# Kernel tuning notes

Measured on AMD Instinct MI355X. Metric: run time of the kernel, lower is better.

## Reference

```python
import jax, jax.numpy as jnp
import numpy as np

N_NODES = 20000
N_EDGES = 120000
N_GRAPHS = 512
F_IN = 300
NHID = 256
NHID_FF = 256
NOUT = 768
SLOPE = 0.2
EPS = 1e-16


def _p(key, shape, scale=0.05):
    return jax.random.normal(key, shape, dtype=jnp.float32) * scale


def setup_inputs() -> dict:
    key = jax.random.key(0)
    ks = jax.random.split(key, 24)
    inp = {
        "x": jax.random.normal(ks[0], (N_NODES, F_IN), dtype=jnp.float32),
        "edge_index": jax.random.randint(ks[1], (2, N_EDGES), 0, N_NODES, dtype=jnp.int64) if False else jax.random.randint(ks[1], (2, N_EDGES), 0, N_NODES).astype(jnp.int32),
        "batch": jnp.sort(jax.random.randint(ks[2], (N_NODES,), 0, N_GRAPHS)).astype(jnp.int32),
        # conv1: in=300 -> heads=4, C=256, concat
        "c1_wl": _p(ks[3], (4 * NHID, F_IN)),
        "c1_wr": _p(ks[4], (4 * NHID, F_IN)),
        "c1_att": _p(ks[5], (4, NHID)),
        "c1_b": jnp.zeros((4 * NHID,), jnp.float32),
        # conv2: in=1024 -> heads=4, C=256, concat
        "c2_wl": _p(ks[6], (4 * NHID, 4 * NHID)),
        "c2_wr": _p(ks[7], (4 * NHID, 4 * NHID)),
        "c2_att": _p(ks[8], (4, NHID)),
        "c2_b": jnp.zeros((4 * NHID,), jnp.float32),
        # conv3: in=1024 -> heads=6, C=256, mean (concat=False)
        "c3_wl": _p(ks[9], (6 * NHID_FF, 4 * NHID)),
        "c3_wr": _p(ks[10], (6 * NHID_FF, 4 * NHID)),
        "c3_att": _p(ks[11], (6, NHID_FF)),
        "c3_b": jnp.zeros((NHID_FF,), jnp.float32),
        # post-process MLP
        "fp1_w": _p(ks[12], (NHID_FF, NHID_FF)),
        "fp1_b": jnp.zeros((NHID_FF,), jnp.float32),
        "fp2_w": _p(ks[13], (NOUT, NHID_FF)),
        "fp2_b": jnp.zeros((NOUT,), jnp.float32),
    }
    return inp


def gatv2(x, src, dst, wl, wr, att, b, concat):
    """GATv2Conv (PyG semantics, eval mode): lin_l on source, lin_r on target,
    score = att . leaky_relu(xl_j + xr_i), segment softmax over dst, aggregate xl_j."""
    n = x.shape[0]
    H, C = att.shape
    xl = (x @ wl.T).reshape(n, H, C)
    xr = (x @ wr.T).reshape(n, H, C)
    s = xl[src] + xr[dst]                                   # [E,H,C] gather
    s = jnp.where(s > 0, s, SLOPE * s)                      # leaky_relu
    scores = jnp.einsum("ehc,hc->eh", s, att)               # [E,H]
    mx = jax.ops.segment_max(scores, dst, num_segments=n)   # [N,H]
    ex = jnp.exp(scores - mx[dst])
    denom = jax.ops.segment_sum(ex, dst, num_segments=n)
    alpha = ex / (denom[dst] + EPS)                         # [E,H]
    out = jax.ops.segment_sum(alpha[:, :, None] * xl[src], dst, num_segments=n)  # [N,H,C]
    out = out.reshape(n, H * C) if concat else out.mean(axis=1)
    return out + b


def reference(x, edge_index, batch, c1_wl, c1_wr, c1_att, c1_b,
              c2_wl, c2_wr, c2_att, c2_b, c3_wl, c3_wr, c3_att, c3_b,
              fp1_w, fp1_b, fp2_w, fp2_b):
    n = x.shape[0]
    # PyG GATv2Conv defaults add_self_loops=True
    loops = jnp.arange(n, dtype=edge_index.dtype)
    src = jnp.concatenate([edge_index[0], loops])
    dst = jnp.concatenate([edge_index[1], loops])

    h = jax.nn.elu(gatv2(x, src, dst, c1_wl, c1_wr, c1_att, c1_b, concat=True))
    h = jax.nn.elu(gatv2(h, src, dst, c2_wl, c2_wr, c2_att, c2_b, concat=True))
    h = gatv2(h, src, dst, c3_wl, c3_wr, c3_att, c3_b, concat=False)

    # F.normalize(p=2, dim=-1), torch eps=1e-12
    norm = jnp.linalg.norm(h, axis=-1, keepdims=True)
    h = h / jnp.maximum(norm, 1e-12)

    # global_mean_pool over `batch`
    sums = jax.ops.segment_sum(h, batch, num_segments=N_GRAPHS)
    cnts = jax.ops.segment_sum(jnp.ones((n,), h.dtype), batch, num_segments=N_GRAPHS)
    pooled = sums / jnp.maximum(cnts, 1.0)[:, None]

    h = jax.nn.relu(pooled @ fp1_w.T + fp1_b)
    return h @ fp2_w.T + fp2_b
```

## Files before the change

kernel.cpp:

```cpp
#include <hip/hip_runtime.h>

typedef _Float16 h16;
typedef _Float16 h16x2 __attribute__((ext_vector_type(2)));
typedef _Float16 h16x4 __attribute__((ext_vector_type(4)));
typedef _Float16 h16x8 __attribute__((ext_vector_type(8)));
typedef float f32x4 __attribute__((ext_vector_type(4)));

static constexpr int NN   = 20000;
static constexpr int NPAD = 20224;
static constexpr int NE0  = 120000;
static constexpr int NE   = 140000;
static constexpr int NG   = 512;
static constexpr int FIN  = 300;
static constexpr int K1P  = 384;
static constexpr int CD   = 256;
static constexpr float SLOPE = 0.2f;

#define GLDS16(gsrc, ldst)                                                              \
  __builtin_amdgcn_global_load_lds(                                                    \
      (const __attribute__((address_space(1))) unsigned int*)(gsrc),                    \
      (__attribute__((address_space(3))) unsigned int*)(ldst), 16, 0, 0)

__global__ __launch_bounds__(256) void fill_x_kernel(const float* __restrict__ x, h16* __restrict__ a1) {
  int r = blockIdx.x;
  for (int c = threadIdx.x; c < K1P; c += 256) {
    float v = (r < NN && c < FIN) ? x[(size_t)r * FIN + c] : 0.f;
    a1[(size_t)r * K1P + c] = (h16)v;
  }
}

__global__ __launch_bounds__(256) void conv_w2_kernel(const float* __restrict__ wl, const float* __restrict__ wr,
                                                      h16* __restrict__ o, int rows, int cols, int colsp) {
  int r = blockIdx.x;
  const float* s = (r < rows) ? (wl + (size_t)r * cols) : (wr + (size_t)(r - rows) * cols);
  for (int c = threadIdx.x; c < colsp; c += 256) {
    float v = (c < cols) ? s[c] : 0.f;
    o[(size_t)r * colsp + c] = (h16)v;
  }
}

__global__ __launch_bounds__(256) void attcvt_kernel(const float* __restrict__ a, h16* __restrict__ o, int n) {
  int i = blockIdx.x * 256 + threadIdx.x;
  if (i < n) o[i] = (h16)a[i];
}

__global__ __launch_bounds__(256) void build_edges_kernel(const int* __restrict__ ei,
                                                          int* __restrict__ src, int* __restrict__ dst) {
  int e = blockIdx.x * 256 + threadIdx.x;
  if (e >= NE) return;
  if (e < NE0) { src[e] = ei[e]; dst[e] = ei[NE0 + e]; }
  else         { src[e] = e - NE0; dst[e] = e - NE0; }
}

__global__ __launch_bounds__(256) void deg_kernel(const int* __restrict__ dst, int* __restrict__ deg) {
  int e = blockIdx.x * 256 + threadIdx.x;
  if (e < NE) atomicAdd(&deg[dst[e]], 1);
}

__global__ __launch_bounds__(1024) void scan_kernel(const int* __restrict__ deg, int* __restrict__ rowptr) {
  __shared__ int b0[1024], b1[1024];
  __shared__ int carry;
  int t = threadIdx.x;
  if (t == 0) carry = 0;
  __syncthreads();
  for (int base = 0; base < NN; base += 1024) {
    int x = (base + t < NN) ? deg[base + t] : 0;
    b0[t] = x;
    __syncthreads();
    int* cur = b0; int* nxt = b1;
    for (int off = 1; off < 1024; off <<= 1) {
      int v = cur[t];
      if (t >= off) v += cur[t - off];
      nxt[t] = v;
      __syncthreads();
      int* tmp = cur; cur = nxt; nxt = tmp;
    }
    if (base + t < NN) rowptr[base + t] = carry + cur[t] - x;
    __syncthreads();
    if (t == 0) carry += cur[1023];
    __syncthreads();
  }
  if (t == 0) rowptr[NN] = carry;
}

__global__ __launch_bounds__(256) void scatter_kernel(const int* __restrict__ src, const int* __restrict__ dst,
                                                      const int* __restrict__ rowptr, int* __restrict__ cursor,
                                                      int* __restrict__ esrc) {
  int e = blockIdx.x * 256 + threadIdx.x;
  if (e >= NE) return;
  int d = dst[e];
  int pos = rowptr[d] + atomicAdd(&cursor[d], 1);
  esrc[pos] = src[e];
}

__global__ __launch_bounds__(512, 2) void gemm256_kernel(const h16* __restrict__ A, const h16* __restrict__ B,
                                                         h16* __restrict__ Co, int K, int Nw, int ntN) {
  __shared__ __align__(16) h16 lds[4 * 16384];
  int nwg = gridDim.x;
  int q = nwg >> 3, r = nwg & 7;
  int xc = blockIdx.x & 7, idx = blockIdx.x >> 3;
  int logical = (xc < r ? xc * (q + 1) : r * (q + 1) + (xc - r) * q) + idx;
  int tm = (logical / ntN) * 256, tn = (logical % ntN) * 256;

  int tid = threadIdx.x;
  int wv = tid >> 6, lane = tid & 63;
  int wm = (wv >> 2) * 128, wn = (wv & 3) * 64;
  int lrow = lane & 15, kq = lane >> 4, lr7 = lrow & 7;

  int rowoff = tid >> 3;
  int ug = ((tid & 7) ^ (rowoff & 7)) * 8;
  int ldsoff = (tid >> 6) * 512;

  const int NT = K >> 6;

  auto STAGE = [&](int buf, int kt) {
#pragma unroll
    for (int j = 0; j < 4; ++j) {
      GLDS16(A + (size_t)(tm + j * 64 + rowoff) * K + kt * 64 + ug,
             &lds[(buf * 2 + 0) * 16384 + j * 4096 + ldsoff]);
      GLDS16(B + (size_t)(tn + j * 64 + rowoff) * K + kt * 64 + ug,
             &lds[(buf * 2 + 1) * 16384 + j * 4096 + ldsoff]);
    }
  };

  STAGE(0, 0);
  STAGE(1, 1);

  f32x4 acc[8][4] = {};
  for (int t = 0; t < NT; ++t) {
    int b = t & 1;
    if (t + 1 < NT) { asm volatile("s_waitcnt vmcnt(8)" ::: "memory"); }
    else            { asm volatile("s_waitcnt vmcnt(0)" ::: "memory"); }
    __builtin_amdgcn_s_barrier();

    const h16* As_ = &lds[(b * 2 + 0) * 16384];
    const h16* Bs_ = &lds[(b * 2 + 1) * 16384];
    h16x8 af[8], bf[4];
#pragma unroll
    for (int i = 0; i < 8; ++i) af[i] = *(const h16x8*)&As_[(wm + i * 16 + lrow) * 64 + ((kq ^ lr7) * 8)];
#pragma unroll
    for (int j = 0; j < 4; ++j) bf[j] = *(const h16x8*)&Bs_[(wn + j * 16 + lrow) * 64 + ((kq ^ lr7) * 8)];
#pragma unroll
    for (int i = 0; i < 8; ++i)
#pragma unroll
      for (int j = 0; j < 4; ++j)
        acc[i][j] = __builtin_amdgcn_mfma_f32_16x16x32_f16(af[i], bf[j], acc[i][j], 0, 0, 0);
#pragma unroll
    for (int i = 0; i < 8; ++i) af[i] = *(const h16x8*)&As_[(wm + i * 16 + lrow) * 64 + (((4 + kq) ^ lr7) * 8)];
#pragma unroll
    for (int j = 0; j < 4; ++j) bf[j] = *(const h16x8*)&Bs_[(wn + j * 16 + lrow) * 64 + (((4 + kq) ^ lr7) * 8)];
    asm volatile("s_waitcnt lgkmcnt(0)" ::: "memory");
    __builtin_amdgcn_sched_barrier(0);
    __builtin_amdgcn_s_barrier();
    if (t + 2 < NT) STAGE(b, t + 2);
    __builtin_amdgcn_s_setprio(1);
#pragma unroll
    for (int i = 0; i < 8; ++i)
#pragma unroll
      for (int j = 0; j < 4; ++j)
        acc[i][j] = __builtin_amdgcn_mfma_f32_16x16x32_f16(af[i], bf[j], acc[i][j], 0, 0, 0);
    __builtin_amdgcn_s_setprio(0);
  }

  int cr = kq * 4, cc = lrow;
#pragma unroll
  for (int i = 0; i < 8; ++i)
#pragma unroll
    for (int j = 0; j < 4; ++j) {
      size_t base = (size_t)(tm + wm + i * 16 + cr) * Nw + (tn + wn + j * 16 + cc);
#pragma unroll
      for (int qq = 0; qq < 4; qq++) Co[base + (size_t)qq * Nw] = (h16)acc[i][j][qq];
    }
}

template <int H, int MODE>
__global__ __launch_bounds__(64 * H) void sagg_kernel(
    const h16* __restrict__ X, const int* __restrict__ rowptr, const int* __restrict__ esrc,
    const h16* __restrict__ attH, const float* __restrict__ bias,
    h16* __restrict__ outA, const int* __restrict__ batch,
    float* __restrict__ pooled, int* __restrict__ cnt) {
  constexpr int NS = H / 2;
  constexpr int HC = H * CD;
  constexpr unsigned ROWB = (unsigned)(4 * HC);
  int tid = threadIdx.x;
  int w = tid >> 6, lane = tid & 63;
  int k = w / NS, s = w - k * NS;
  int n = blockIdx.x * 2 + k;
  unsigned sby = (unsigned)s * 1024u + (unsigned)lane * 16u;
  const char* Xb = (const char*)X;
  unsigned nrow = (unsigned)n * ROWB;

  h16x8 xr8 = *(const h16x8*)(Xb + nrow + (unsigned)(2 * HC) + sby);
  h16x8 aw8 = *(const h16x8*)((const char*)attH + sby);
  int beg = rowptr[n], end = rowptr[n + 1];

  float m = -1e30f, den = 0.f;
  float acc[8] = {0.f, 0.f, 0.f, 0.f, 0.f, 0.f, 0.f, 0.f};

  for (int i = beg; i < end; i += 8) {
    int cn = end - i; if (cn > 8) cn = 8;
    unsigned offs[8];
#pragma unroll
    for (int kk = 0; kk < 8; ++kk) {
      int idx = i + kk; if (idx > end - 1) idx = end - 1;
      offs[kk] = (unsigned)esrc[idx] * ROWB + sby;
    }
    h16x8 xv[8];
#pragma unroll
    for (int kk = 0; kk < 8; ++kk) xv[kk] = *(const h16x8*)(Xb + offs[kk]);
    float ps[8];
#pragma unroll
    for (int kk = 0; kk < 8; ++kk) {
      h16x8 v = xv[kk] + xr8;
      h16x8 u = v * (h16)SLOPE;
      v = __builtin_elementwise_max(v, u);
      float p = 0.f;
      p = __builtin_amdgcn_fdot2(__builtin_shufflevector(v, v, 0, 1),
                                 __builtin_shufflevector(aw8, aw8, 0, 1), p, false);
      p = __builtin_amdgcn_fdot2(__builtin_shufflevector(v, v, 2, 3),
                                 __builtin_shufflevector(aw8, aw8, 2, 3), p, false);
      p = __builtin_amdgcn_fdot2(__builtin_shufflevector(v, v, 4, 5),
                                 __builtin_shufflevector(aw8, aw8, 4, 5), p, false);
      p = __builtin_amdgcn_fdot2(__builtin_shufflevector(v, v, 6, 7),
                                 __builtin_shufflevector(aw8, aw8, 6, 7), p, false);
      p += __shfl_xor(p, 1);  p += __shfl_xor(p, 2);  p += __shfl_xor(p, 4);
      p += __shfl_xor(p, 8);  p += __shfl_xor(p, 16);
      ps[kk] = p;
    }
    float pm = ps[0];
#pragma unroll
    for (int kk = 1; kk < 8; ++kk) pm = fmaxf(pm, ps[kk]);
    float nm = fmaxf(m, pm);
    float f = __expf(m - nm);
    den *= f;
#pragma unroll
    for (int j = 0; j < 8; ++j) acc[j] *= f;
#pragma unroll
    for (int kk = 0; kk < 8; ++kk) {
      float we = (kk < cn) ? __expf(ps[kk] - nm) : 0.f;
      den += we;
#pragma unroll
      for (int j = 0; j < 8; ++j) acc[j] += we * (float)xv[kk][j];
    }
    m = nm;
  }
  float inv = 1.f / (den + 1e-16f);

  if (MODE == 0) {
    const float* bp = bias + s * 512 + lane * 8;
    float4 b0 = *(const float4*)bp;
    float4 b1 = *(const float4*)(bp + 4);
    const float* bb = (const float*)&b0;
    const float* bb2 = (const float*)&b1;
    h16x8 ov;
#pragma unroll
    for (int j = 0; j < 8; ++j) {
      float o = acc[j] * inv + (j < 4 ? bb[j] : bb2[j - 4]);
      o = o > 0.f ? o : expm1f(o);
      ov[j] = (h16)o;
    }
    *(h16x8*)(outA + (unsigned)n * HC + s * 512 + lane * 8) = ov;
  } else {
    __shared__ float sacc[2][NS][32][8];
    __shared__ float spart[2][2 * NS];
    float t8[8];
#pragma unroll
    for (int j = 0; j < 8; ++j) {
      t8[j] = acc[j] * inv;
      t8[j] += __shfl_xor(t8[j], 32);
    }
    if (lane < 32) {
#pragma unroll
      for (int j = 0; j < 8; ++j) sacc[k][s][lane][j] = t8[j];
    }
    __syncthreads();
#pragma unroll
    for (int kk = 0; kk < 2; ++kk) {
      float mv = 0.f;
      if (tid < CD) {
#pragma unroll
        for (int s2 = 0; s2 < NS; ++s2) mv += sacc[kk][s2][tid >> 3][tid & 7];
        mv = mv * (1.f / H) + bias[tid];
      }
      float ss = (tid < CD) ? mv * mv : 0.f;
      ss += __shfl_xor(ss, 1);  ss += __shfl_xor(ss, 2);  ss += __shfl_xor(ss, 4);
      ss += __shfl_xor(ss, 8);  ss += __shfl_xor(ss, 16); ss += __shfl_xor(ss, 32);
      if (lane == 0) spart[kk][w] = ss;
      __syncthreads();
      float tot = 0.f;
#pragma unroll
      for (int ww = 0; ww < 2 * NS; ++ww) tot += spart[kk][ww];
      float scale = 1.f / fmaxf(sqrtf(tot), 1e-12f);
      int g = batch[blockIdx.x * 2 + kk];
      if (tid < CD) atomicAdd(&pooled[(unsigned)g * CD + tid], mv * scale);
      if (tid == 0) atomicAdd(&cnt[g], 1);
    }
  }
}

__global__ __launch_bounds__(256) void pool_div_kernel(float* __restrict__ pooled, const int* __restrict__ cnt) {
  int g = blockIdx.x, t = threadIdx.x;
  pooled[(size_t)g * CD + t] /= fmaxf((float)cnt[g], 1.f);
}

__global__ __launch_bounds__(256) void mlp1_kernel(const float* __restrict__ pooled, const float* __restrict__ w,
                                                   const float* __restrict__ b, float* __restrict__ hid) {
  __shared__ float xs[CD];
  int g = blockIdx.x, t = threadIdx.x;
  xs[t] = pooled[(size_t)g * CD + t];
  __syncthreads();
  float acc = b[t];
  for (int k = 0; k < CD; ++k) acc += xs[k] * w[(size_t)t * CD + k];
  hid[(size_t)g * CD + t] = fmaxf(acc, 0.f);
}

__global__ __launch_bounds__(256) void mlp2_kernel(const float* __restrict__ hid, const float* __restrict__ w,
                                                   const float* __restrict__ b, float* __restrict__ out) {
  __shared__ float xs[CD];
  int g = blockIdx.x, t = threadIdx.x;
  xs[t] = hid[(size_t)g * CD + t];
  __syncthreads();
  for (int o = t; o < 768; o += 256) {
    float acc = b[o];
    for (int k = 0; k < CD; ++k) acc += xs[k] * w[(size_t)o * CD + k];
    out[(size_t)g * 768 + o] = acc;
  }
}

extern "C" void kernel_launch(void* const* d_in, const int* in_sizes, int n_in,
                              void* d_out, int out_size, void* d_ws, size_t ws_size,
                              hipStream_t stream) {
  const float* x      = (const float*)d_in[0];
  const int*   ei     = (const int*)d_in[1];
  const int*   batch  = (const int*)d_in[2];
  const float* c1_wl  = (const float*)d_in[3];
  const float* c1_wr  = (const float*)d_in[4];
  const float* c1_att = (const float*)d_in[5];
  const float* c1_b   = (const float*)d_in[6];
  const float* c2_wl  = (const float*)d_in[7];
  const float* c2_wr  = (const float*)d_in[8];
  const float* c2_att = (const float*)d_in[9];
  const float* c2_b   = (const float*)d_in[10];
  const float* c3_wl  = (const float*)d_in[11];
  const float* c3_wr  = (const float*)d_in[12];
  const float* c3_att = (const float*)d_in[13];
  const float* c3_b   = (const float*)d_in[14];
  const float* fp1_w  = (const float*)d_in[15];
  const float* fp1_b  = (const float*)d_in[16];
  const float* fp2_w  = (const float*)d_in[17];
  const float* fp2_b  = (const float*)d_in[18];

  char* p = (char*)d_ws;
  size_t off = 0;
  auto alloc = [&](size_t b) { void* r = p + off; off += (b + 255) & ~(size_t)255; return r; };
  h16*  A    = (h16*)alloc((size_t)NPAD * 1024 * 2);
  h16*  Xa   = (h16*)alloc((size_t)NPAD * 3072 * 2);
  h16*  Xb   = (h16*)alloc((size_t)NPAD * 2048 * 2);
  h16*  A1   = Xb;
  h16*  W1   = (h16*)alloc((size_t)2048 * K1P * 2);
  h16*  W2   = (h16*)alloc((size_t)2048 * 1024 * 2);
  h16*  W3   = (h16*)alloc((size_t)3072 * 1024 * 2);
  h16*  attH1 = (h16*)alloc((size_t)4 * CD * 2);
  h16*  attH2 = (h16*)alloc((size_t)4 * CD * 2);
  h16*  attH3 = (h16*)alloc((size_t)6 * CD * 2);
  int*  srcA   = (int*)alloc((size_t)NE * 4);
  int*  dstA   = (int*)alloc((size_t)NE * 4);
  int*  esrc   = (int*)alloc((size_t)NE * 4);
  int*  deg    = (int*)alloc((size_t)NN * 4);
  int*  cursor = (int*)alloc((size_t)NN * 4);
  int*  rowptr = (int*)alloc((size_t)(NN + 1) * 4);
  float* pooled = (float*)alloc((size_t)NG * CD * 4);
  int*  cnt    = (int*)alloc((size_t)NG * 4);
  float* hid   = (float*)alloc((size_t)NG * CD * 4);

  hipMemsetAsync(deg, 0, (size_t)NN * 4, stream);
  hipMemsetAsync(cursor, 0, (size_t)NN * 4, stream);
  hipMemsetAsync(pooled, 0, (size_t)NG * CD * 4, stream);
  hipMemsetAsync(cnt, 0, (size_t)NG * 4, stream);

  fill_x_kernel<<<NPAD, 256, 0, stream>>>(x, A1);
  conv_w2_kernel<<<2048, 256, 0, stream>>>(c1_wl, c1_wr, W1, 1024, FIN, K1P);
  conv_w2_kernel<<<2048, 256, 0, stream>>>(c2_wl, c2_wr, W2, 1024, 1024, 1024);
  conv_w2_kernel<<<3072, 256, 0, stream>>>(c3_wl, c3_wr, W3, 1536, 1024, 1024);
  attcvt_kernel<<<4, 256, 0, stream>>>(c1_att, attH1, 4 * CD);
  attcvt_kernel<<<4, 256, 0, stream>>>(c2_att, attH2, 4 * CD);
  attcvt_kernel<<<6, 256, 0, stream>>>(c3_att, attH3, 6 * CD);

  int eb = (NE + 255) / 256;
  build_edges_kernel<<<eb, 256, 0, stream>>>(ei, srcA, dstA);
  deg_kernel<<<eb, 256, 0, stream>>>(dstA, deg);
  scan_kernel<<<1, 1024, 0, stream>>>(deg, rowptr);
  scatter_kernel<<<eb, 256, 0, stream>>>(srcA, dstA, rowptr, cursor, esrc);

  int sb = NN / 2;

  gemm256_kernel<<<79 * 8, 512, 0, stream>>>(A1, W1, Xa, K1P, 2048, 8);
  sagg_kernel<4, 0><<<sb, 256, 0, stream>>>(Xa, rowptr, esrc, attH1, c1_b, A, nullptr, nullptr, nullptr);

  gemm256_kernel<<<79 * 8, 512, 0, stream>>>(A, W2, Xb, 1024, 2048, 8);
  sagg_kernel<4, 0><<<sb, 256, 0, stream>>>(Xb, rowptr, esrc, attH2, c2_b, A, nullptr, nullptr, nullptr);

  gemm256_kernel<<<79 * 12, 512, 0, stream>>>(A, W3, Xa, 1024, 3072, 12);
  sagg_kernel<6, 1><<<sb, 384, 0, stream>>>(Xa, rowptr, esrc, attH3, c3_b, nullptr, batch, pooled, cnt);

  pool_div_kernel<<<NG, 256, 0, stream>>>(pooled, cnt);
  mlp1_kernel<<<NG, 256, 0, stream>>>(pooled, fp1_w, fp1_b, hid);
  mlp2_kernel<<<NG, 256, 0, stream>>>(hid, fp2_w, fp2_b, (float*)d_out);
}
```

Baseline: 782.2 us.

## Split GATv2 aggregation into separate score, softmax, and weighted-sum kernels

```diff
diff --git a/kernel.cpp b/kernel.cpp
--- a/kernel.cpp
+++ b/kernel.cpp
@@ -85,12 +85,13 @@
 
 __global__ __launch_bounds__(256) void scatter_kernel(const int* __restrict__ src, const int* __restrict__ dst,
                                                       const int* __restrict__ rowptr, int* __restrict__ cursor,
-                                                      int* __restrict__ esrc) {
+                                                      int* __restrict__ esrc, int* __restrict__ edst) {
   int e = blockIdx.x * 256 + threadIdx.x;
   if (e >= NE) return;
   int d = dst[e];
   int pos = rowptr[d] + atomicAdd(&cursor[d], 1);
   esrc[pos] = src[e];
+  edst[pos] = d;
 }
 
 __global__ __launch_bounds__(512, 2) void gemm256_kernel(const h16* __restrict__ A, const h16* __restrict__ B,
@@ -173,12 +174,76 @@
     }
 }
 
+__device__ inline float dot16(h16x8 v0, h16x8 v1, h16x8 w0, h16x8 w1, float p) {
+  p = __builtin_amdgcn_fdot2(__builtin_shufflevector(v0, v0, 0, 1), __builtin_shufflevector(w0, w0, 0, 1), p, false);
+  p = __builtin_amdgcn_fdot2(__builtin_shufflevector(v0, v0, 2, 3), __builtin_shufflevector(w0, w0, 2, 3), p, false);
+  p = __builtin_amdgcn_fdot2(__builtin_shufflevector(v0, v0, 4, 5), __builtin_shufflevector(w0, w0, 4, 5), p, false);
+  p = __builtin_amdgcn_fdot2(__builtin_shufflevector(v0, v0, 6, 7), __builtin_shufflevector(w0, w0, 6, 7), p, false);
+  p = __builtin_amdgcn_fdot2(__builtin_shufflevector(v1, v1, 0, 1), __builtin_shufflevector(w1, w1, 0, 1), p, false);
+  p = __builtin_amdgcn_fdot2(__builtin_shufflevector(v1, v1, 2, 3), __builtin_shufflevector(w1, w1, 2, 3), p, false);
+  p = __builtin_amdgcn_fdot2(__builtin_shufflevector(v1, v1, 4, 5), __builtin_shufflevector(w1, w1, 4, 5), p, false);
+  p = __builtin_amdgcn_fdot2(__builtin_shufflevector(v1, v1, 6, 7), __builtin_shufflevector(w1, w1, 6, 7), p, false);
+  return p;
+}
+
+template <int H>
+__global__ __launch_bounds__(256) void score_kernel(
+    const h16* __restrict__ X, const int* __restrict__ esrc, const int* __restrict__ edst,
+    const h16* __restrict__ attH, float* __restrict__ sc) {
+  constexpr int HC = H * CD;
+  constexpr unsigned ROWB = (unsigned)(4 * HC);
+  int i = blockIdx.x * 16 + (threadIdx.x >> 4);
+  if (i >= NE) return;
+  int g = threadIdx.x & 15;
+  unsigned go = (unsigned)g * 32u;
+  const char* Xb = (const char*)X;
+  const char* Ab = (const char*)attH;
+  unsigned xlb = (unsigned)esrc[i] * ROWB + go;
+  unsigned xrb = (unsigned)edst[i] * ROWB + (unsigned)(2 * HC) + go;
+  float ps[H];
+#pragma unroll
+  for (int h = 0; h < H; ++h) {
+    unsigned off = (unsigned)h * 512u;
+    h16x8 a0 = *(const h16x8*)(Xb + xlb + off);
+    h16x8 a1 = *(const h16x8*)(Xb + xlb + off + 16u);
+    h16x8 b0 = *(const h16x8*)(Xb + xrb + off);
+    h16x8 b1 = *(const h16x8*)(Xb + xrb + off + 16u);
+    h16x8 w0 = *(const h16x8*)(Ab + off + go);
+    h16x8 w1 = *(const h16x8*)(Ab + off + go + 16u);
+    h16x8 v0 = a0 + b0, v1 = a1 + b1;
+    h16x8 u0 = v0 * (h16)SLOPE, u1 = v1 * (h16)SLOPE;
+    v0 = __builtin_elementwise_max(v0, u0);
+    v1 = __builtin_elementwise_max(v1, u1);
+    float p = dot16(v0, v1, w0, w1, 0.f);
+    p += __shfl_xor(p, 1); p += __shfl_xor(p, 2);
+    p += __shfl_xor(p, 4); p += __shfl_xor(p, 8);
+    ps[h] = p;
+  }
+  if (g == 0) {
+#pragma unroll
+    for (int h = 0; h < H; ++h) sc[(size_t)i * H + h] = ps[h];
+  }
+}
+
+template <int H>
+__global__ __launch_bounds__(256) void smax_kernel(const int* __restrict__ rowptr, float* __restrict__ sc) {
+  int t = blockIdx.x * 256 + threadIdx.x;
+  int n = t / H, h = t - n * H;
+  if (n >= NN) return;
+  int beg = rowptr[n], end = rowptr[n + 1];
+  float m = -1e30f;
+  for (int i = beg; i < end; ++i) m = fmaxf(m, sc[(size_t)i * H + h]);
+  float den = 0.f;
+  for (int i = beg; i < end; ++i) den += __expf(sc[(size_t)i * H + h] - m);
+  float inv = 1.f / (den + 1e-16f);
+  for (int i = beg; i < end; ++i) sc[(size_t)i * H + h] = __expf(sc[(size_t)i * H + h] - m) * inv;
+}
+
 template <int H, int MODE>
-__global__ __launch_bounds__(64 * H) void sagg_kernel(
+__global__ __launch_bounds__(64 * H) void agg_kernel(
     const h16* __restrict__ X, const int* __restrict__ rowptr, const int* __restrict__ esrc,
-    const h16* __restrict__ attH, const float* __restrict__ bias,
-    h16* __restrict__ outA, const int* __restrict__ batch,
-    float* __restrict__ pooled, int* __restrict__ cnt) {
+    const float* __restrict__ sc, const float* __restrict__ bias,
+    h16* __restrict__ outA, float* __restrict__ Fb3) {
   constexpr int NS = H / 2;
   constexpr int HC = H * CD;
   constexpr unsigned ROWB = (unsigned)(4 * HC);
@@ -187,64 +252,30 @@
   int k = w / NS, s = w - k * NS;
   int n = blockIdx.x * 2 + k;
   unsigned sby = (unsigned)s * 1024u + (unsigned)lane * 16u;
+  int hsel = 2 * s + (lane >> 5);
   const char* Xb = (const char*)X;
-  unsigned nrow = (unsigned)n * ROWB;
-
-  h16x8 xr8 = *(const h16x8*)(Xb + nrow + (unsigned)(2 * HC) + sby);
-  h16x8 aw8 = *(const h16x8*)((const char*)attH + sby);
   int beg = rowptr[n], end = rowptr[n + 1];
 
-  float m = -1e30f, den = 0.f;
   float acc[8] = {0.f, 0.f, 0.f, 0.f, 0.f, 0.f, 0.f, 0.f};
-
   for (int i = beg; i < end; i += 8) {
-    int cn = end - i; if (cn > 8) cn = 8;
     unsigned offs[8];
+    float al[8];
 #pragma unroll
     for (int kk = 0; kk < 8; ++kk) {
-      int idx = i + kk; if (idx > end - 1) idx = end - 1;
+      int idx = i + kk;
+      bool ok = idx < end;
+      if (!ok) idx = end - 1;
       offs[kk] = (unsigned)esrc[idx] * ROWB + sby;
+      al[kk] = ok ? sc[(size_t)idx * H + hsel] : 0.f;
     }
     h16x8 xv[8];
 #pragma unroll
     for (int kk = 0; kk < 8; ++kk) xv[kk] = *(const h16x8*)(Xb + offs[kk]);
-    float ps[8];
-#pragma unroll
-    for (int kk = 0; kk < 8; ++kk) {
-      h16x8 v = xv[kk] + xr8;
-      h16x8 u = v * (h16)SLOPE;
-      v = __builtin_elementwise_max(v, u);
-      float p = 0.f;
-      p = __builtin_amdgcn_fdot2(__builtin_shufflevector(v, v, 0, 1),
-                                 __builtin_shufflevector(aw8, aw8, 0, 1), p, false);
-      p = __builtin_amdgcn_fdot2(__builtin_shufflevector(v, v, 2, 3),
-                                 __builtin_shufflevector(aw8, aw8, 2, 3), p, false);
-      p = __builtin_amdgcn_fdot2(__builtin_shufflevector(v, v, 4, 5),
-                                 __builtin_shufflevector(aw8, aw8, 4, 5), p, false);
-      p = __builtin_amdgcn_fdot2(__builtin_shufflevector(v, v, 6, 7),
-                                 __builtin_shufflevector(aw8, aw8, 6, 7), p, false);
-      p += __shfl_xor(p, 1);  p += __shfl_xor(p, 2);  p += __shfl_xor(p, 4);
-      p += __shfl_xor(p, 8);  p += __shfl_xor(p, 16);
-      ps[kk] = p;
-    }
-    float pm = ps[0];
-#pragma unroll
-    for (int kk = 1; kk < 8; ++kk) pm = fmaxf(pm, ps[kk]);
-    float nm = fmaxf(m, pm);
-    float f = __expf(m - nm);
-    den *= f;
-#pragma unroll
-    for (int j = 0; j < 8; ++j) acc[j] *= f;
-#pragma unroll
-    for (int kk = 0; kk < 8; ++kk) {
-      float we = (kk < cn) ? __expf(ps[kk] - nm) : 0.f;
-      den += we;
-#pragma unroll
-      for (int j = 0; j < 8; ++j) acc[j] += we * (float)xv[kk][j];
-    }
-    m = nm;
-  }
-  float inv = 1.f / (den + 1e-16f);
+#pragma unroll
+    for (int kk = 0; kk < 8; ++kk)
+#pragma unroll
+      for (int j = 0; j < 8; ++j) acc[j] += al[kk] * (float)xv[kk][j];
+  }
 
   if (MODE == 0) {
     const float* bp = bias + s * 512 + lane * 8;
@@ -255,47 +286,50 @@
     h16x8 ov;
 #pragma unroll
     for (int j = 0; j < 8; ++j) {
-      float o = acc[j] * inv + (j < 4 ? bb[j] : bb2[j - 4]);
+      float o = acc[j] + (j < 4 ? bb[j] : bb2[j - 4]);
       o = o > 0.f ? o : expm1f(o);
       ov[j] = (h16)o;
     }
     *(h16x8*)(outA + (unsigned)n * HC + s * 512 + lane * 8) = ov;
   } else {
-    __shared__ float sacc[2][NS][32][8];
-    __shared__ float spart[2][2 * NS];
     float t8[8];
 #pragma unroll
     for (int j = 0; j < 8; ++j) {
-      t8[j] = acc[j] * inv;
+      t8[j] = acc[j];
       t8[j] += __shfl_xor(t8[j], 32);
     }
     if (lane < 32) {
-#pragma unroll
-      for (int j = 0; j < 8; ++j) sacc[k][s][lane][j] = t8[j];
-    }
-    __syncthreads();
-#pragma unroll
-    for (int kk = 0; kk < 2; ++kk) {
-      float mv = 0.f;
-      if (tid < CD) {
-#pragma unroll
-        for (int s2 = 0; s2 < NS; ++s2) mv += sacc[kk][s2][tid >> 3][tid & 7];
-        mv = mv * (1.f / H) + bias[tid];
-      }
-      float ss = (tid < CD) ? mv * mv : 0.f;
-      ss += __shfl_xor(ss, 1);  ss += __shfl_xor(ss, 2);  ss += __shfl_xor(ss, 4);
-      ss += __shfl_xor(ss, 8);  ss += __shfl_xor(ss, 16); ss += __shfl_xor(ss, 32);
-      if (lane == 0) spart[kk][w] = ss;
-      __syncthreads();
-      float tot = 0.f;
-#pragma unroll
-      for (int ww = 0; ww < 2 * NS; ++ww) tot += spart[kk][ww];
-      float scale = 1.f / fmaxf(sqrtf(tot), 1e-12f);
-      int g = batch[blockIdx.x * 2 + kk];
-      if (tid < CD) atomicAdd(&pooled[(unsigned)g * CD + tid], mv * scale);
-      if (tid == 0) atomicAdd(&cnt[g], 1);
-    }
-  }
+      float* dst = Fb3 + ((size_t)n * NS + s) * CD + lane * 8;
+      float4 o0 = {t8[0], t8[1], t8[2], t8[3]};
+      float4 o1 = {t8[4], t8[5], t8[6], t8[7]};
+      *(float4*)dst = o0;
+      *(float4*)(dst + 4) = o1;
+    }
+  }
+}
+
+template <int H>
+__global__ __launch_bounds__(256) void normpool_kernel(const float* __restrict__ Fb3,
+                                                       const float* __restrict__ bias,
+                                                       const int* __restrict__ batch,
+                                                       float* __restrict__ pooled, int* __restrict__ cnt) {
+  constexpr int NS = H / 2;
+  int n = blockIdx.x, t = threadIdx.x;
+  float mv = 0.f;
+#pragma unroll
+  for (int s = 0; s < NS; ++s) mv += Fb3[((size_t)n * NS + s) * CD + t];
+  mv = mv * (1.f / H) + bias[t];
+  float ss = mv * mv;
+  ss += __shfl_xor(ss, 1);  ss += __shfl_xor(ss, 2);  ss += __shfl_xor(ss, 4);
+  ss += __shfl_xor(ss, 8);  ss += __shfl_xor(ss, 16); ss += __shfl_xor(ss, 32);
+  __shared__ float ws4[4];
+  if ((t & 63) == 0) ws4[t >> 6] = ss;
+  __syncthreads();
+  float tot = ws4[0] + ws4[1] + ws4[2] + ws4[3];
+  float scale = 1.f / fmaxf(sqrtf(tot), 1e-12f);
+  int g = batch[n];
+  atomicAdd(&pooled[(size_t)g * CD + t], mv * scale);
+  if (t == 0) atomicAdd(&cnt[g], 1);
 }
 
 __global__ __launch_bounds__(256) void pool_div_kernel(float* __restrict__ pooled, const int* __restrict__ cnt) {
@@ -357,15 +391,18 @@
   h16*  Xa   = (h16*)alloc((size_t)NPAD * 3072 * 2);
   h16*  Xb   = (h16*)alloc((size_t)NPAD * 2048 * 2);
   h16*  A1   = Xb;
+  float* Fb3 = (float*)Xb;
   h16*  W1   = (h16*)alloc((size_t)2048 * K1P * 2);
   h16*  W2   = (h16*)alloc((size_t)2048 * 1024 * 2);
   h16*  W3   = (h16*)alloc((size_t)3072 * 1024 * 2);
   h16*  attH1 = (h16*)alloc((size_t)4 * CD * 2);
   h16*  attH2 = (h16*)alloc((size_t)4 * CD * 2);
   h16*  attH3 = (h16*)alloc((size_t)6 * CD * 2);
+  float* sc   = (float*)alloc((size_t)NE * 6 * 4);
   int*  srcA   = (int*)alloc((size_t)NE * 4);
   int*  dstA   = (int*)alloc((size_t)NE * 4);
   int*  esrc   = (int*)alloc((size_t)NE * 4);
+  int*  edst   = (int*)alloc((size_t)NE * 4);
   int*  deg    = (int*)alloc((size_t)NN * 4);
   int*  cursor = (int*)alloc((size_t)NN * 4);
   int*  rowptr = (int*)alloc((size_t)(NN + 1) * 4);
@@ -390,18 +427,23 @@
   build_edges_kernel<<<eb, 256, 0, stream>>>(ei, srcA, dstA);
   deg_kernel<<<eb, 256, 0, stream>>>(dstA, deg);
   scan_kernel<<<1, 1024, 0, stream>>>(deg, rowptr);
-  scatter_kernel<<<eb, 256, 0, stream>>>(srcA, dstA, rowptr, cursor, esrc);
-
-  int sb = NN / 2;
+  scatter_kernel<<<eb, 256, 0, stream>>>(srcA, dstA, rowptr, cursor, esrc, edst);
 
   gemm256_kernel<<<79 * 8, 512, 0, stream>>>(A1, W1, Xa, K1P, 2048, 8);
-  sagg_kernel<4, 0><<<sb, 256, 0, stream>>>(Xa, rowptr, esrc, attH1, c1_b, A, nullptr, nullptr, nullptr);
+  score_kernel<4><<<NE / 16, 256, 0, stream>>>(Xa, esrc, edst, attH1, sc);
+  smax_kernel<4><<<(NN * 4 + 255) / 256, 256, 0, stream>>>(rowptr, sc);
+  agg_kernel<4, 0><<<NN / 2, 256, 0, stream>>>(Xa, rowptr, esrc, sc, c1_b, A, nullptr);
 
   gemm256_kernel<<<79 * 8, 512, 0, stream>>>(A, W2, Xb, 1024, 2048, 8);
-  sagg_kernel<4, 0><<<sb, 256, 0, stream>>>(Xb, rowptr, esrc, attH2, c2_b, A, nullptr, nullptr, nullptr);
+  score_kernel<4><<<NE / 16, 256, 0, stream>>>(Xb, esrc, edst, attH2, sc);
+  smax_kernel<4><<<(NN * 4 + 255) / 256, 256, 0, stream>>>(rowptr, sc);
+  agg_kernel<4, 0><<<NN / 2, 256, 0, stream>>>(Xb, rowptr, esrc, sc, c2_b, A, nullptr);
 
   gemm256_kernel<<<79 * 12, 512, 0, stream>>>(A, W3, Xa, 1024, 3072, 12);
-  sagg_kernel<6, 1><<<sb, 384, 0, stream>>>(Xa, rowptr, esrc, attH3, c3_b, nullptr, batch, pooled, cnt);
+  score_kernel<6><<<NE / 16, 256, 0, stream>>>(Xa, esrc, edst, attH3, sc);
+  smax_kernel<6><<<(NN * 6 + 255) / 256, 256, 0, stream>>>(rowptr, sc);
+  agg_kernel<6, 1><<<NN / 2, 384, 0, stream>>>(Xa, rowptr, esrc, sc, nullptr, nullptr, Fb3);
+  normpool_kernel<6><<<NN, 256, 0, stream>>>(Fb3, c3_b, batch, pooled, cnt);
 
   pool_div_kernel<<<NG, 256, 0, stream>>>(pooled, cnt);
   mlp1_kernel<<<NG, 256, 0, stream>>>(pooled, fp1_w, fp1_b, hid);
```

After: 834.2 us. 1.07x slower.

## Decouple GAT aggregation warps from node blocks and split conv3 norm-pool into separate kernel

Applied to the files above, without the earlier changes.

```diff
diff --git a/kernel.cpp b/kernel.cpp
--- a/kernel.cpp
+++ b/kernel.cpp
@@ -174,73 +174,64 @@
 }
 
 template <int H, int MODE>
-__global__ __launch_bounds__(64 * H) void sagg_kernel(
+__global__ __launch_bounds__(256, 4) void sagg_kernel(
     const h16* __restrict__ X, const int* __restrict__ rowptr, const int* __restrict__ esrc,
     const h16* __restrict__ attH, const float* __restrict__ bias,
-    h16* __restrict__ outA, const int* __restrict__ batch,
-    float* __restrict__ pooled, int* __restrict__ cnt) {
+    h16* __restrict__ outA, float* __restrict__ Fb3) {
   constexpr int NS = H / 2;
   constexpr int HC = H * CD;
   constexpr unsigned ROWB = (unsigned)(4 * HC);
-  int tid = threadIdx.x;
-  int w = tid >> 6, lane = tid & 63;
-  int k = w / NS, s = w - k * NS;
-  int n = blockIdx.x * 2 + k;
+  int flat = blockIdx.x * 4 + (threadIdx.x >> 6);
+  if (flat >= NN * NS) return;
+  int n = flat / NS, s = flat - n * NS;
+  int lane = threadIdx.x & 63;
   unsigned sby = (unsigned)s * 1024u + (unsigned)lane * 16u;
   const char* Xb = (const char*)X;
-  unsigned nrow = (unsigned)n * ROWB;
-
-  h16x8 xr8 = *(const h16x8*)(Xb + nrow + (unsigned)(2 * HC) + sby);
+
+  h16x8 xr8 = *(const h16x8*)(Xb + (unsigned)n * ROWB + (unsigned)(2 * HC) + sby);
   h16x8 aw8 = *(const h16x8*)((const char*)attH + sby);
   int beg = rowptr[n], end = rowptr[n + 1];
 
   float m = -1e30f, den = 0.f;
   float acc[8] = {0.f, 0.f, 0.f, 0.f, 0.f, 0.f, 0.f, 0.f};
 
-  for (int i = beg; i < end; i += 8) {
-    int cn = end - i; if (cn > 8) cn = 8;
-    unsigned offs[8];
-#pragma unroll
-    for (int kk = 0; kk < 8; ++kk) {
-      int idx = i + kk; if (idx > end - 1) idx = end - 1;
-      offs[kk] = (unsigned)esrc[idx] * ROWB + sby;
-    }
-    h16x8 xv[8];
-#pragma unroll
-    for (int kk = 0; kk < 8; ++kk) xv[kk] = *(const h16x8*)(Xb + offs[kk]);
-    float ps[8];
-#pragma unroll
-    for (int kk = 0; kk < 8; ++kk) {
-      h16x8 v = xv[kk] + xr8;
+  for (int i = beg; i < end; i += 16) {
+    int cn = end - i; if (cn > 16) cn = 16;
+    h16x8 xv[16];
+#pragma unroll
+    for (int k = 0; k < 16; ++k) {
+      int idx = i + k; if (idx >= end) idx = end - 1;
+      xv[k] = *(const h16x8*)(Xb + (unsigned)esrc[idx] * ROWB + sby);
+    }
+    float ps[16];
+#pragma unroll
+    for (int k = 0; k < 16; ++k) {
+      h16x8 v = xv[k] + xr8;
       h16x8 u = v * (h16)SLOPE;
       v = __builtin_elementwise_max(v, u);
       float p = 0.f;
-      p = __builtin_amdgcn_fdot2(__builtin_shufflevector(v, v, 0, 1),
-                                 __builtin_shufflevector(aw8, aw8, 0, 1), p, false);
-      p = __builtin_amdgcn_fdot2(__builtin_shufflevector(v, v, 2, 3),
-                                 __builtin_shufflevector(aw8, aw8, 2, 3), p, false);
-      p = __builtin_amdgcn_fdot2(__builtin_shufflevector(v, v, 4, 5),
-                                 __builtin_shufflevector(aw8, aw8, 4, 5), p, false);
-      p = __builtin_amdgcn_fdot2(__builtin_shufflevector(v, v, 6, 7),
-                                 __builtin_shufflevector(aw8, aw8, 6, 7), p, false);
+      p = __builtin_amdgcn_fdot2(__builtin_shufflevector(v, v, 0, 1), __builtin_shufflevector(aw8, aw8, 0, 1), p, false);
+      p = __builtin_amdgcn_fdot2(__builtin_shufflevector(v, v, 2, 3), __builtin_shufflevector(aw8, aw8, 2, 3), p, false);
+      p = __builtin_amdgcn_fdot2(__builtin_shufflevector(v, v, 4, 5), __builtin_shufflevector(aw8, aw8, 4, 5), p, false);
+      p = __builtin_amdgcn_fdot2(__builtin_shufflevector(v, v, 6, 7), __builtin_shufflevector(aw8, aw8, 6, 7), p, false);
       p += __shfl_xor(p, 1);  p += __shfl_xor(p, 2);  p += __shfl_xor(p, 4);
       p += __shfl_xor(p, 8);  p += __shfl_xor(p, 16);
-      ps[kk] = p;
+      ps[k] = p;
     }
     float pm = ps[0];
 #pragma unroll
-    for (int kk = 1; kk < 8; ++kk) pm = fmaxf(pm, ps[kk]);
+    for (int k = 1; k < 16; ++k) pm = fmaxf(pm, ps[k]);
     float nm = fmaxf(m, pm);
     float f = __expf(m - nm);
     den *= f;
 #pragma unroll
     for (int j = 0; j < 8; ++j) acc[j] *= f;
 #pragma unroll
-    for (int kk = 0; kk < 8; ++kk) {
-      float we = (kk < cn) ? __expf(ps[kk] - nm) : 0.f;
+    for (int k = 0; k < 16; ++k) {
+      float we = (k < cn) ? __expf(ps[k] - nm) : 0.f;
       den += we;
 #pragma unroll
-      for (int j = 0; j < 8; ++j) acc[j] += we * (float)xv[kk][j];
+      for (int j = 0; j < 8; ++j) acc[j] += we * (float)xv[k][j];
     }
     m = nm;
   }
@@ -261,8 +252,6 @@
     }
     *(h16x8*)(outA + (unsigned)n * HC + s * 512 + lane * 8) = ov;
   } else {
-    __shared__ float sacc[2][NS][32][8];
-    __shared__ float spart[2][2 * NS];
     float t8[8];
 #pragma unroll
     for (int j = 0; j < 8; ++j) {
@@ -270,32 +259,37 @@
       t8[j] += __shfl_xor(t8[j], 32);
     }
     if (lane < 32) {
-#pragma unroll
-      for (int j = 0; j < 8; ++j) sacc[k][s][lane][j] = t8[j];
-    }
-    __syncthreads();
-#pragma unroll
-    for (int kk = 0; kk < 2; ++kk) {
-      float mv = 0.f;
-      if (tid < CD) {
-#pragma unroll
-        for (int s2 = 0; s2 < NS; ++s2) mv += sacc[kk][s2][tid >> 3][tid & 7];
-        mv = mv * (1.f / H) + bias[tid];
-      }
-      float ss = (tid < CD) ? mv * mv : 0.f;
-      ss += __shfl_xor(ss, 1);  ss += __shfl_xor(ss, 2);  ss += __shfl_xor(ss, 4);
-      ss += __shfl_xor(ss, 8);  ss += __shfl_xor(ss, 16); ss += __shfl_xor(ss, 32);
-      if (lane == 0) spart[kk][w] = ss;
-      __syncthreads();
-      float tot = 0.f;
-#pragma unroll
-      for (int ww = 0; ww < 2 * NS; ++ww) tot += spart[kk][ww];
-      float scale = 1.f / fmaxf(sqrtf(tot), 1e-12f);
-      int g = batch[blockIdx.x * 2 + kk];
-      if (tid < CD) atomicAdd(&pooled[(unsigned)g * CD + tid], mv * scale);
-      if (tid == 0) atomicAdd(&cnt[g], 1);
-    }
-  }
+      float* dst = Fb3 + ((unsigned)n * NS + s) * CD + lane * 8;
+      float4 o0 = {t8[0], t8[1], t8[2], t8[3]};
+      float4 o1 = {t8[4], t8[5], t8[6], t8[7]};
+      *(float4*)dst = o0;
+      *(float4*)(dst + 4) = o1;
+    }
+  }
+}
+
+template <int H>
+__global__ __launch_bounds__(256) void normpool_kernel(const float* __restrict__ Fb3,
+                                                       const float* __restrict__ bias,
+                                                       const int* __restrict__ batch,
+                                                       float* __restrict__ pooled, int* __restrict__ cnt) {
+  constexpr int NS = H / 2;
+  int n = blockIdx.x, t = threadIdx.x;
+  float mv = 0.f;
+#pragma unroll
+  for (int s = 0; s < NS; ++s) mv += Fb3[((size_t)n * NS + s) * CD + t];
+  mv = mv * (1.f / H) + bias[t];
+  float ss = mv * mv;
+  ss += __shfl_xor(ss, 1);  ss += __shfl_xor(ss, 2);  ss += __shfl_xor(ss, 4);
+  ss += __shfl_xor(ss, 8);  ss += __shfl_xor(ss, 16); ss += __shfl_xor(ss, 32);
+  __shared__ float ws4[4];
+  if ((t & 63) == 0) ws4[t >> 6] = ss;
+  __syncthreads();
+  float tot = ws4[0] + ws4[1] + ws4[2] + ws4[3];
+  float scale = 1.f / fmaxf(sqrtf(tot), 1e-12f);
+  int g = batch[n];
+  atomicAdd(&pooled[(size_t)g * CD + t], mv * scale);
+  if (t == 0) atomicAdd(&cnt[g], 1);
 }
 
 __global__ __launch_bounds__(256) void pool_div_kernel(float* __restrict__ pooled, const int* __restrict__ cnt) {
@@ -357,6 +351,7 @@
   h16*  Xa   = (h16*)alloc((size_t)NPAD * 3072 * 2);
   h16*  Xb   = (h16*)alloc((size_t)NPAD * 2048 * 2);
   h16*  A1   = Xb;
+  float* Fb3 = (float*)Xb;
   h16*  W1   = (h16*)alloc((size_t)2048 * K1P * 2);
   h16*  W2   = (h16*)alloc((size_t)2048 * 1024 * 2);
   h16*  W3   = (h16*)alloc((size_t)3072 * 1024 * 2);
@@ -392,16 +387,15 @@
   scan_kernel<<<1, 1024, 0, stream>>>(deg, rowptr);
   scatter_kernel<<<eb, 256, 0, stream>>>(srcA, dstA, rowptr, cursor, esrc);
 
-  int sb = NN / 2;
-
   gemm256_kernel<<<79 * 8, 512, 0, stream>>>(A1, W1, Xa, K1P, 2048, 8);
-  sagg_kernel<4, 0><<<sb, 256, 0, stream>>>(Xa, rowptr, esrc, attH1, c1_b, A, nullptr, nullptr, nullptr);
+  sagg_kernel<4, 0><<<NN * 2 / 4, 256, 0, stream>>>(Xa, rowptr, esrc, attH1, c1_b, A, nullptr);
 
   gemm256_kernel<<<79 * 8, 512, 0, stream>>>(A, W2, Xb, 1024, 2048, 8);
-  sagg_kernel<4, 0><<<sb, 256, 0, stream>>>(Xb, rowptr, esrc, attH2, c2_b, A, nullptr, nullptr, nullptr);
+  sagg_kernel<4, 0><<<NN * 2 / 4, 256, 0, stream>>>(Xb, rowptr, esrc, attH2, c2_b, A, nullptr);
 
   gemm256_kernel<<<79 * 12, 512, 0, stream>>>(A, W3, Xa, 1024, 3072, 12);
-  sagg_kernel<6, 1><<<sb, 384, 0, stream>>>(Xa, rowptr, esrc, attH3, c3_b, nullptr, batch, pooled, cnt);
+  sagg_kernel<6, 1><<<NN * 3 / 4, 256, 0, stream>>>(Xa, rowptr, esrc, attH3, nullptr, nullptr, Fb3);
+  normpool_kernel<6><<<NN, 256, 0, stream>>>(Fb3, c3_b, batch, pooled, cnt);
 
   pool_div_kernel<<<NG, 256, 0, stream>>>(pooled, cnt);
   mlp1_kernel<<<NG, 256, 0, stream>>>(pooled, fp1_w, fp1_b, hid);
```

Result: slower. 878.9 us (+12.4%).
